# Optimization experiments

Measured on AMD Instinct MI355X. Metric: run time of the kernel, lower is better.

## Reference

```python
import jax, jax.numpy as jnp
import numpy as np

SOS_TOKEN = 0
HIDDEN = 512
EMBED = 256
V_SRC = 32000
V_TGT = 50257
S_LEN = 512
T_LEN = 512


def setup_inputs() -> dict:
    key = jax.random.key(0)
    ks = jax.random.split(key, 16)
    s = 0.02
    return {
        "source": jax.random.randint(ks[0], (S_LEN,), 0, V_SRC),
        "target": jax.random.randint(ks[1], (T_LEN, 1), 0, V_TGT),
        "emb_e": jax.random.normal(ks[2], (V_SRC, EMBED), jnp.float32) * s,
        "Wih_e": jax.random.normal(ks[3], (3 * HIDDEN, EMBED), jnp.float32) * s,
        "Whh_e": jax.random.normal(ks[4], (3 * HIDDEN, HIDDEN), jnp.float32) * s,
        "bih_e": jax.random.normal(ks[5], (3 * HIDDEN,), jnp.float32) * s,
        "bhh_e": jax.random.normal(ks[6], (3 * HIDDEN,), jnp.float32) * s,
        "emb_d": jax.random.normal(ks[7], (V_TGT, EMBED), jnp.float32) * s,
        "Wih_d": jax.random.normal(ks[8], (3 * HIDDEN, EMBED), jnp.float32) * s,
        "Whh_d": jax.random.normal(ks[9], (3 * HIDDEN, HIDDEN), jnp.float32) * s,
        "bih_d": jax.random.normal(ks[10], (3 * HIDDEN,), jnp.float32) * s,
        "bhh_d": jax.random.normal(ks[11], (3 * HIDDEN,), jnp.float32) * s,
        "Wout": jax.random.normal(ks[12], (V_TGT, HIDDEN), jnp.float32) * s,
        "bout": jax.random.normal(ks[13], (V_TGT,), jnp.float32) * s,
    }


def _gru_step(h, x, Wih, Whh, bih, bhh):
    # PyTorch GRU cell: gates ordered (r, z, n)
    gi = Wih @ x + bih            # [3H]
    gh = Whh @ h + bhh            # [3H]
    gi_r, gi_z, gi_n = jnp.split(gi, 3)
    gh_r, gh_z, gh_n = jnp.split(gh, 3)
    r = jax.nn.sigmoid(gi_r + gh_r)
    z = jax.nn.sigmoid(gi_z + gh_z)
    n = jnp.tanh(gi_n + r * gh_n)
    return (1.0 - z) * n + z * h


def reference(source, target, emb_e, Wih_e, Whh_e, bih_e, bhh_e,
              emb_d, Wih_d, Whh_d, bih_d, bhh_d, Wout, bout):
    # Encoder (faithful to original: gru called per-token with zero hidden,
    # so only the last source token determines encoder_hidden).
    x_last = emb_e[source[-1]]                       # [E]
    h0 = jnp.zeros((HIDDEN,), dtype=emb_e.dtype)
    h_enc = _gru_step(h0, x_last, Wih_e, Whh_e, bih_e, bhh_e)  # [H]

    # Decoder with teacher forcing (ratio=1.0): inputs are SOS, target[:-1]
    tgt = target[:, 0]
    tokens = jnp.concatenate([jnp.array([SOS_TOKEN], dtype=tgt.dtype), tgt[:-1]])

    def step(h, tok):
        x = jax.nn.relu(emb_d[tok])                  # [E]
        h2 = _gru_step(h, x, Wih_d, Whh_d, bih_d, bhh_d)
        logp = jax.nn.log_softmax(Wout @ h2 + bout)  # [V]
        return h2, logp

    _, logps = jax.lax.scan(step, h_enc, tokens)     # [T, V]
    return logps[:, None, :]                         # [T, 1, V]
```

## Files before the change

kernel.cpp:

```cpp
#include <hip/hip_runtime.h>
#include <stdint.h>

#define HIDDEN 512
#define EMBED  256
#define VTGT   50257
#define TLEN   512
#define GATE3  1536
#define REC_B  16
#define GEMM_B 224
#define NBLK   (REC_B + GEMM_B)
#define NJT    ((VTGT + 127) / 128)

typedef float f32x4 __attribute__((ext_vector_type(4)));
typedef unsigned int u32;
typedef unsigned int u32x4 __attribute__((ext_vector_type(4)));

__device__ __forceinline__ unsigned short f2bf(float f) {
  union { float f; unsigned u; } v; v.f = f;
  unsigned u = v.u;
  unsigned r = (u + 0x7FFFu + ((u >> 16) & 1u)) >> 16;
  return (unsigned short)r;
}

__device__ __forceinline__ float sigm(float x) {
  return __builtin_amdgcn_rcpf(1.f + __expf(-x));
}
__device__ __forceinline__ float fast_tanh(float x) {
  return 1.f - 2.f * __builtin_amdgcn_rcpf(__expf(2.f * x) + 1.f);
}

__device__ __forceinline__ u32 cpoll(const u32* p) {
  u32 v;
  asm volatile("global_load_dword %0, %1, off sc0 sc1\n\ts_waitcnt vmcnt(0)"
               : "=v"(v) : "v"(p) : "memory");
  return v;
}
__device__ __forceinline__ void cload4x4(const u32* p, u32x4& a, u32x4& b,
                                         u32x4& c, u32x4& d) {
  asm volatile(
      "global_load_dwordx4 %0, %4, off sc0 sc1\n\t"
      "global_load_dwordx4 %1, %4, off offset:16 sc0 sc1\n\t"
      "global_load_dwordx4 %2, %4, off offset:32 sc0 sc1\n\t"
      "global_load_dwordx4 %3, %4, off offset:48 sc0 sc1\n\t"
      "s_waitcnt vmcnt(0)"
      : "=v"(a), "=v"(b), "=v"(c), "=v"(d) : "v"(p) : "memory");
}
__device__ __forceinline__ void cload2(const u32* p0, const u32* p1,
                                       u32x4& a, u32x4& b) {
  asm volatile(
      "global_load_dwordx4 %0, %2, off sc0 sc1\n\t"
      "global_load_dwordx4 %1, %3, off sc0 sc1\n\t"
      "s_waitcnt vmcnt(0)"
      : "=v"(a), "=v"(b) : "v"(p0), "v"(p1) : "memory");
}
__device__ __forceinline__ void cstore(u32* p, u32 v) {
  asm volatile("global_store_dword %0, %1, off sc0 sc1" :: "v"(p), "v"(v) : "memory");
}
__device__ __forceinline__ void cstore4(u32* p, u32x4 v) {
  asm volatile("global_store_dwordx4 %0, %1, off sc0 sc1" :: "v"(p), "v"(v) : "memory");
}
__device__ __forceinline__ void cload2_l(const u32* p0, const u32* p1,
                                         u32x4& a, u32x4& b) {
  asm volatile(
      "global_load_dwordx4 %0, %2, off sc0\n\t"
      "global_load_dwordx4 %1, %3, off sc0\n\t"
      "s_waitcnt vmcnt(0)"
      : "=v"(a), "=v"(b) : "v"(p0), "v"(p1) : "memory");
}
__device__ __forceinline__ void cstore4_l(u32* p, u32x4 v) {
  asm volatile("global_store_dwordx4 %0, %1, off sc0" :: "v"(p), "v"(v) : "memory");
}

__global__ void kenc1(const int* source, const float* emb_e, const float* Wih_e,
                      const float* bih_e, float* genc) {
  __shared__ float xs[EMBED];
  int tid = threadIdx.x;
  int tok = source[511];
  if (tid < EMBED) xs[tid] = emb_e[(size_t)tok * EMBED + tid];
  __syncthreads();
  int j = blockIdx.x * 256 + tid;
  const float* w = Wih_e + (size_t)j * EMBED;
  float acc = bih_e[j];
  for (int k = 0; k < EMBED; k += 4) {
    float4 wv = *(const float4*)(w + k);
    acc += wv.x * xs[k] + wv.y * xs[k + 1] + wv.z * xs[k + 2] + wv.w * xs[k + 3];
  }
  genc[j] = acc;
}

__global__ void kenc2(const float* genc, const float* bhh_e, u32* hs, u32* hsm) {
  int e = threadIdx.x;
  float r = sigm(genc[e] + bhh_e[e]);
  float z = sigm(genc[e + 512] + bhh_e[e + 512]);
  float n = tanhf(genc[e + 1024] + r * bhh_e[e + 1024]);
  float h = (1.f - z) * n;
  u32 pk = (__float_as_uint(h) & ~511u) | 256u;
  hs[e] = pk;
  hsm[e] = pk;
}

__global__ __launch_bounds__(256) void kgi(const int* target, const float* emb_d,
                                           const float* Wih_d, const float* bih_d,
                                           float* GI) {
  __shared__ float Xs[32][EMBED];
  int tid = threadIdx.x;
  int j0 = blockIdx.x * 128;
  int t0 = blockIdx.y * 32;
  for (int idx = tid; idx < 32 * EMBED; idx += 256) {
    int tt = idx >> 8, c = idx & 255;
    int t = t0 + tt;
    int tok = (t == 0) ? 0 : target[t - 1];
    float v = emb_d[(size_t)tok * EMBED + c];
    Xs[tt][c] = v > 0.f ? v : 0.f;
  }
  __syncthreads();
  int jl = tid & 127, tg = tid >> 7;
  int j = j0 + jl;
  const float* w = Wih_d + (size_t)j * EMBED;
  float acc[16];
#pragma unroll
  for (int i = 0; i < 16; ++i) acc[i] = 0.f;
  for (int k = 0; k < EMBED; k += 4) {
    float4 wv = *(const float4*)(w + k);
#pragma unroll
    for (int i = 0; i < 16; ++i) {
      int tl = tg * 16 + i;
      acc[i] += wv.x * Xs[tl][k] + wv.y * Xs[tl][k + 1] +
                wv.z * Xs[tl][k + 2] + wv.w * Xs[tl][k + 3];
    }
  }
  float b = bih_d[j];
#pragma unroll
  for (int i = 0; i < 16; ++i) {
    int t = t0 + tg * 16 + i;
    GI[(size_t)t * GATE3 + j] = acc[i] + b;
  }
}

#define DOT4(w, h) (w[0]*h[0] + w[1]*h[1] + w[2]*h[2] + w[3]*h[3])

__device__ void rec_path(int slot, const float* __restrict__ Whh,
                         const float* __restrict__ bhh,
                         const float* __restrict__ GI, u32* hs, u32* hsm,
                         u32* stepv, char* SM) {
  int tid = threadIdx.x;
  int p = tid & 15, r = tid >> 4;
  int e = slot * 32 + r;
  int k0 = p * 32;
  float* hbuf = (float*)SM;
  const f32x4* Wr = (const f32x4*)(Whh + (size_t)e * HIDDEN + k0);
  const f32x4* Wz = (const f32x4*)(Whh + (size_t)(e + 512) * HIDDEN + k0);
  const f32x4* Wn = (const f32x4*)(Whh + (size_t)(e + 1024) * HIDDEN + k0);
  f32x4 wr0 = Wr[0], wr1 = Wr[1], wr2 = Wr[2], wr3 = Wr[3],
        wr4 = Wr[4], wr5 = Wr[5], wr6 = Wr[6], wr7 = Wr[7];
  f32x4 wz0 = Wz[0], wz1 = Wz[1], wz2 = Wz[2], wz3 = Wz[3],
        wz4 = Wz[4], wz5 = Wz[5], wz6 = Wz[6], wz7 = Wz[7];
  f32x4 wn0 = Wn[0], wn1 = Wn[1], wn2 = Wn[2], wn3 = Wn[3],
        wn4 = Wn[4], wn5 = Wn[5], wn6 = Wn[6], wn7 = Wn[7];
  float br = bhh[e], bz = bhh[e + 512], bn = bhh[e + 1024];
  float hold = __uint_as_float(hs[e] & ~511u);
  __builtin_amdgcn_s_setprio(1);
  int lane = tid & 63;
  int d0 = lane * 4;
  int i0 = ((d0 >> 5) * 36) + (d0 & 31);
  int i1 = (((d0 + 256) >> 5) * 36) + (d0 & 31);
  int w = tid >> 6;
  u32* pub_l = hs + slot * 32 + w * 4;
  u32* pub_m = hsm + slot * 32 + w * 4;
  int fb = 0;
  for (int t = 0; t < TLEN; ++t) {
    int par = t & 1;
    float gie = 0.f, giz = 0.f, gin = 0.f;
    if (p == 0) {
      const float* git = GI + (size_t)t * GATE3;
      gie = git[e]; giz = git[e + 512]; gin = git[e + 1024];
    }
    if (tid < 128) {
      const u32* s0 = hs + (size_t)t * HIDDEN + d0;
      const u32* s1 = s0 + 256;
      u32 want = 256u + ((u32)t & 255u);
      u32x4 a, b;
      bool ok = false;
      int tries = (fb >= 8) ? 0 : 24;
      for (int it = 0; it < tries && !ok; ++it) {
        cload2_l(s0, s1, a, b);
        u32 bad = 0;
#pragma unroll
        for (int q = 0; q < 4; ++q) bad |= (a[q] ^ want) | (b[q] ^ want);
        ok = !__any((bad & 511u) != 0u);
      }
      if (!ok) {
        ++fb;
        const u32* m0 = hsm + (size_t)t * HIDDEN + d0;
        const u32* m1 = m0 + 256;
        do {
          cload2(m0, m1, a, b);
          u32 bad = 0;
#pragma unroll
          for (int q = 0; q < 4; ++q) bad |= (a[q] ^ want) | (b[q] ^ want);
          ok = !__any((bad & 511u) != 0u);
        } while (!ok);
      }
      f32x4 fa, fc;
#pragma unroll
      for (int q = 0; q < 4; ++q) {
        fa[q] = __uint_as_float(a[q] & ~511u);
        fc[q] = __uint_as_float(b[q] & ~511u);
      }
      *(f32x4*)&hbuf[par * 576 + i0] = fa;
      *(f32x4*)&hbuf[par * 576 + i1] = fc;
    }
    __syncthreads();
    if (slot == 0 && tid == 128) cstore(stepv, (u32)t);
    const f32x4* hp4 = (const f32x4*)(hbuf + par * 576 + p * 36);
    f32x4 h0 = hp4[0], h1 = hp4[1], h2 = hp4[2], h3 = hp4[3],
          h4 = hp4[4], h5 = hp4[5], h6 = hp4[6], h7 = hp4[7];
    float pr = DOT4(wr0, h0) + DOT4(wr1, h1) + DOT4(wr2, h2) + DOT4(wr3, h3) +
               DOT4(wr4, h4) + DOT4(wr5, h5) + DOT4(wr6, h6) + DOT4(wr7, h7);
    float pz = DOT4(wz0, h0) + DOT4(wz1, h1) + DOT4(wz2, h2) + DOT4(wz3, h3) +
               DOT4(wz4, h4) + DOT4(wz5, h5) + DOT4(wz6, h6) + DOT4(wz7, h7);
    float pn = DOT4(wn0, h0) + DOT4(wn1, h1) + DOT4(wn2, h2) + DOT4(wn3, h3) +
               DOT4(wn4, h4) + DOT4(wn5, h5) + DOT4(wn6, h6) + DOT4(wn7, h7);
#pragma unroll
    for (int m = 1; m < 16; m <<= 1) {
      pr += __shfl_xor(pr, m);
      pz += __shfl_xor(pz, m);
      pn += __shfl_xor(pn, m);
    }
    u32 pk = 0;
    if (p == 0) {
      float rg = sigm(gie + pr + br);
      float z  = sigm(giz + pz + bz);
      float n  = fast_tanh(gin + rg * (pn + bn));
      float hnew = (1.f - z) * n + z * hold;
      hold = hnew;
      pk = (__float_as_uint(hnew) & ~511u) | (256u + ((u32)(t + 1) & 255u));
    }
    u32x4 o;
    o[0] = __shfl(pk, 0);  o[1] = __shfl(pk, 16);
    o[2] = __shfl(pk, 32); o[3] = __shfl(pk, 48);
    if ((tid & 63) == 0) {
      cstore4_l(pub_l + (size_t)(t + 1) * HIDDEN, o);
      cstore4(pub_m + (size_t)(t + 1) * HIDDEN, o);
    }
  }
  if (slot == 0 && tid < 64) {
    const u32* m0 = hsm + (size_t)TLEN * HIDDEN + d0;
    const u32* m1 = m0 + 256;
    u32 want = 256u + ((u32)TLEN & 255u);
    u32x4 a, b;
    for (;;) {
      cload2(m0, m1, a, b);
      u32 bad = 0;
#pragma unroll
      for (int q = 0; q < 4; ++q) bad |= (a[q] ^ want) | (b[q] ^ want);
      if (!__any((bad & 511u) != 0u)) break;
    }
    if (tid == 0) cstore(stepv, (u32)TLEN);
  }
}

__device__ void gemm_path(int g, const u32* hsm, u32* stepv, const float* Wout,
                          const float* bout, float* rs, float* out, char* SM) {
  unsigned short* As = (unsigned short*)SM;
  float* rsum = (float*)(SM + 64 * 520 * 2);
  int tid = threadIdx.x;
  int w = tid >> 6, lane = tid & 63;
  int jl = lane & 15, kq = lane >> 4;
  int srow = tid >> 3, scg = tid & 7;
  if (tid < 64) rsum[tid] = 0.f;
  for (int t0i = 0; t0i < 8; ++t0i) {
    int t0 = t0i * 64;
    if (tid == 0) {
      while ((int)cpoll(stepv) < t0 + 64) __builtin_amdgcn_s_sleep(16);
    }
    __syncthreads();
    int slot = t0 + srow + 1;
    u32 want = 256u + ((u32)slot & 255u);
    const u32* sbase = hsm + (size_t)slot * HIDDEN + scg * 64;
#pragma unroll
    for (int b = 0; b < 4; ++b) {
      const u32* sp = sbase + b * 16;
      u32x4 c0, c1, c2, c3;
      for (;;) {
        cload4x4(sp, c0, c1, c2, c3);
        u32 bad = 0;
#pragma unroll
        for (int q = 0; q < 4; ++q)
          bad |= (c0[q] ^ want) | (c1[q] ^ want) | (c2[q] ^ want) | (c3[q] ^ want);
        if (!(bad & 511u)) break;
      }
      u32 dw[8];
#pragma unroll
      for (int q = 0; q < 4; ++q) {
        u32x4 cq = (q == 0) ? c0 : (q == 1) ? c1 : (q == 2) ? c2 : c3;
        float f0 = __uint_as_float(cq[0] & ~511u);
        float f1 = __uint_as_float(cq[1] & ~511u);
        float f2 = __uint_as_float(cq[2] & ~511u);
        float f3 = __uint_as_float(cq[3] & ~511u);
        dw[q * 2]     = (u32)f2bf(f0) | ((u32)f2bf(f1) << 16);
        dw[q * 2 + 1] = (u32)f2bf(f2) | ((u32)f2bf(f3) << 16);
      }
      *(u32x4*)&As[srow * 520 + scg * 64 + b * 16]     = *(u32x4*)&dw[0];
      *(u32x4*)&As[srow * 520 + scg * 64 + b * 16 + 8] = *(u32x4*)&dw[4];
    }
    __syncthreads();
    for (int jt = g; jt < NJT; jt += GEMM_B) {
      int j = jt * 128 + w * 16 + jl;
      int jc = j < VTGT ? j : VTGT - 1;
      const float* Bp = Wout + (size_t)jc * HIDDEN + kq * 8;
      f32x4 acc[4];
#pragma unroll
      for (int i = 0; i < 4; ++i) acc[i] = (f32x4)(0.f);
#pragma unroll
      for (int ks = 0; ks < 16; ++ks) {
        float4 b0 = *(const float4*)(Bp + ks * 32);
        float4 b1 = *(const float4*)(Bp + ks * 32 + 4);
        u32x4 bf;
        bf[0] = (u32)f2bf(b0.x) | ((u32)f2bf(b0.y) << 16);
        bf[1] = (u32)f2bf(b0.z) | ((u32)f2bf(b0.w) << 16);
        bf[2] = (u32)f2bf(b1.x) | ((u32)f2bf(b1.y) << 16);
        bf[3] = (u32)f2bf(b1.z) | ((u32)f2bf(b1.w) << 16);
#pragma unroll
        for (int tq = 0; tq < 4; ++tq) {
          u32x4 af = *(const u32x4*)&As[(tq * 16 + jl) * 520 + ks * 32 + kq * 8];
          asm volatile("v_mfma_f32_16x16x32_bf16 %0, %1, %2, %0"
                       : "+v"(acc[tq]) : "v"(af), "v"(bf));
        }
      }
      asm volatile("s_nop 7\n\ts_nop 7\n\ts_nop 7" ::);
      bool jok = j < VTGT;
      float bj = jok ? bout[j] : 0.f;
#pragma unroll
      for (int tq = 0; tq < 4; ++tq) {
#pragma unroll
        for (int rr = 0; rr < 4; ++rr) {
          int t = t0 + tq * 16 + kq * 4 + rr;
          float lg = acc[tq][rr] + bj;
          if (jok) out[(size_t)t * VTGT + j] = lg;
          float ex = jok ? __expf(lg) : 0.f;
#pragma unroll
          for (int m = 1; m < 16; m <<= 1) ex += __shfl_xor(ex, m);
          if (jl == 0) atomicAdd(&rsum[tq * 16 + kq * 4 + rr], ex);
        }
      }
    }
    __syncthreads();
    if (tid < 64) {
      atomicAdd(rs + t0 + tid, rsum[tid]);
      rsum[tid] = 0.f;
    }
  }
}

__global__ __launch_bounds__(512, 2) void kmain(const float* Whh, const float* bhh,
                                                const float* GI, u32* hs, u32* hsm,
                                                u32* stepv, u32* ctl,
                                                const float* Wout, const float* bout,
                                                float* rs, float* out) {
  __shared__ __align__(16) char SM[64 * 520 * 2 + 256];
  __shared__ int role;
  int tid = threadIdx.x;
  if (tid == 0) {
    u32 xcc;
    asm volatile("s_getreg_b32 %0, hwreg(HW_REG_XCC_ID)" : "=s"(xcc));
    xcc &= 7u;
    u32 myt = __hip_atomic_fetch_add(&ctl[xcc], 1u, __ATOMIC_RELAXED,
                                     __HIP_MEMORY_SCOPE_AGENT);
    __hip_atomic_fetch_add(&ctl[8], 1u, __ATOMIC_RELEASE, __HIP_MEMORY_SCOPE_AGENT);
    while (__hip_atomic_load(&ctl[8], __ATOMIC_ACQUIRE, __HIP_MEMORY_SCOPE_AGENT)
           < (u32)NBLK)
      __builtin_amdgcn_s_sleep(8);
    int rx = 0;
    for (int x = 0; x < 8; ++x) {
      u32 c = __hip_atomic_load(&ctl[x], __ATOMIC_RELAXED, __HIP_MEMORY_SCOPE_AGENT);
      if (c >= (u32)REC_B) { rx = x; break; }
    }
    if ((int)xcc == rx && myt < (u32)REC_B) {
      role = (int)myt;
    } else {
      role = -1 - (int)__hip_atomic_fetch_add(&ctl[9], 1u, __ATOMIC_RELAXED,
                                              __HIP_MEMORY_SCOPE_AGENT);
    }
  }
  __syncthreads();
  int rl = role;
  if (rl >= 0) rec_path(rl, Whh, bhh, GI, hs, hsm, stepv, SM);
  else gemm_path(-1 - rl, hsm, stepv, Wout, bout, rs, out, SM);
}

__global__ __launch_bounds__(1024) void klsub(float* out, const float* rs) {
  int t = blockIdx.x;
  float l = logf(rs[t]);
  float* row = out + (size_t)t * VTGT;
  for (int jj = threadIdx.x; jj < VTGT; jj += 1024) row[jj] -= l;
}

extern "C" void kernel_launch(void* const* d_in, const int* in_sizes, int n_in,
                              void* d_out, int out_size, void* d_ws, size_t ws_size,
                              hipStream_t stream) {
  const int*   source = (const int*)d_in[0];
  const int*   target = (const int*)d_in[1];
  const float* emb_e  = (const float*)d_in[2];
  const float* Wih_e  = (const float*)d_in[3];
  const float* bih_e  = (const float*)d_in[5];
  const float* bhh_e  = (const float*)d_in[6];
  const float* emb_d  = (const float*)d_in[7];
  const float* Wih_d  = (const float*)d_in[8];
  const float* Whh_d  = (const float*)d_in[9];
  const float* bih_d  = (const float*)d_in[10];
  const float* bhh_d  = (const float*)d_in[11];
  const float* Wout   = (const float*)d_in[12];
  const float* bout   = (const float*)d_in[13];
  float* out = (float*)d_out;
  char* ws = (char*)d_ws;

  float* GI    = (float*)(ws + 0);
  u32*   hs    = (u32*)(ws + 3145728);
  u32*   hsm   = (u32*)(ws + 4196352);
  u32*   stepv = (u32*)(ws + 5246976);
  float* rs    = (float*)(ws + 5247104);
  u32*   ctl   = (u32*)(ws + 5249152);
  float* genc  = (float*)(ws + 5249280);

  hipMemsetAsync(ws + 3145728, 0, 2103552, stream);
  kenc1<<<6, 256, 0, stream>>>(source, emb_e, Wih_e, bih_e, genc);
  kenc2<<<1, 512, 0, stream>>>(genc, bhh_e, hs, hsm);
  kgi<<<dim3(12, 16), 256, 0, stream>>>(target, emb_d, Wih_d, bih_d, GI);
  kmain<<<NBLK, 512, 0, stream>>>(Whh_d, bhh_d, GI, hs, hsm, stepv, ctl,
                                  Wout, bout, rs, out);
  klsub<<<512, 1024, 0, stream>>>(out, rs);
}
```

Measured before the change: 859.6 us.

## Publish hidden state with per-lane dword stores, throttle step counter, vectorize log-subtract

In the recurrent loop, the four-lane shuffle and the single-lane dwordx4 publish are replaced by direct per-lane dword stores: p==0 lanes write the local copy and p==1 lanes write the coherent copy. This takes the shuffles and the one-lane store off the critical path. The global step counter is now written only every 64 steps, which cuts coherent store traffic but may delay consumers that poll it. The final log-subtract kernel uses float4 accesses on rows that are not 16-byte aligned for odd t, plus a scalar tail.

```diff
diff --git a/kernel.cpp b/kernel.cpp
--- a/kernel.cpp
+++ b/kernel.cpp
@@ -56,9 +56,6 @@
 __device__ __forceinline__ void cstore(u32* p, u32 v) {
   asm volatile("global_store_dword %0, %1, off sc0 sc1" :: "v"(p), "v"(v) : "memory");
 }
-__device__ __forceinline__ void cstore4(u32* p, u32x4 v) {
-  asm volatile("global_store_dwordx4 %0, %1, off sc0 sc1" :: "v"(p), "v"(v) : "memory");
-}
 __device__ __forceinline__ void cload2_l(const u32* p0, const u32* p1,
                                          u32x4& a, u32x4& b) {
   asm volatile(
@@ -67,8 +64,8 @@
       "s_waitcnt vmcnt(0)"
       : "=v"(a), "=v"(b) : "v"(p0), "v"(p1) : "memory");
 }
-__device__ __forceinline__ void cstore4_l(u32* p, u32x4 v) {
-  asm volatile("global_store_dwordx4 %0, %1, off sc0" :: "v"(p), "v"(v) : "memory");
+__device__ __forceinline__ void cstore_l(u32* p, u32 v) {
+  asm volatile("global_store_dword %0, %1, off sc0" :: "v"(p), "v"(v) : "memory");
 }
 
 __global__ void kenc1(const int* source, const float* emb_e, const float* Wih_e,
@@ -164,9 +161,6 @@
   int d0 = lane * 4;
   int i0 = ((d0 >> 5) * 36) + (d0 & 31);
   int i1 = (((d0 + 256) >> 5) * 36) + (d0 & 31);
-  int w = tid >> 6;
-  u32* pub_l = hs + slot * 32 + w * 4;
-  u32* pub_m = hsm + slot * 32 + w * 4;
   int fb = 0;
   for (int t = 0; t < TLEN; ++t) {
     int par = t & 1;
@@ -211,7 +205,7 @@
       *(f32x4*)&hbuf[par * 576 + i1] = fc;
     }
     __syncthreads();
-    if (slot == 0 && tid == 128) cstore(stepv, (u32)t);
+    if (slot == 0 && tid == 128 && (t & 63) == 0) cstore(stepv, (u32)t);
     const f32x4* hp4 = (const f32x4*)(hbuf + par * 576 + p * 36);
     f32x4 h0 = hp4[0], h1 = hp4[1], h2 = hp4[2], h3 = hp4[3],
           h4 = hp4[4], h5 = hp4[5], h6 = hp4[6], h7 = hp4[7];
@@ -236,13 +230,10 @@
       hold = hnew;
       pk = (__float_as_uint(hnew) & ~511u) | (256u + ((u32)(t + 1) & 255u));
     }
-    u32x4 o;
-    o[0] = __shfl(pk, 0);  o[1] = __shfl(pk, 16);
-    o[2] = __shfl(pk, 32); o[3] = __shfl(pk, 48);
-    if ((tid & 63) == 0) {
-      cstore4_l(pub_l + (size_t)(t + 1) * HIDDEN, o);
-      cstore4(pub_m + (size_t)(t + 1) * HIDDEN, o);
-    }
+    u32 pkb = __shfl(pk, tid & 48);
+    size_t poff = (size_t)(t + 1) * HIDDEN + e;
+    if (p == 0) cstore_l(hs + poff, pk);
+    else if (p == 1) cstore(hsm + poff, pkb);
   }
   if (slot == 0 && tid < 64) {
     const u32* m0 = hsm + (size_t)TLEN * HIDDEN + d0;
@@ -393,7 +384,14 @@
   int t = blockIdx.x;
   float l = logf(rs[t]);
   float* row = out + (size_t)t * VTGT;
-  for (int jj = threadIdx.x; jj < VTGT; jj += 1024) row[jj] -= l;
+  int tid = threadIdx.x;
+  for (int q = tid; q < 12564; q += 1024) {
+    float4* p = (float4*)(row + q * 4);
+    float4 v = *p;
+    v.x -= l; v.y -= l; v.z -= l; v.w -= l;
+    *p = v;
+  }
+  if (tid == 0) row[VTGT - 1] -= l;
 }
 
 extern "C" void kernel_launch(void* const* d_in, const int* in_sizes, int n_in,
```

Result: no change. 869.3 us (+1.1%).
